# Optimization experiments

Measured on AMD Instinct MI355X. Metric: run time of the kernel, lower is better.

The kernel has to match this reference:

```python
import jax, jax.numpy as jnp
import numpy as np

B, N = 2, 512
D_NODE, D_EDGE, D_HID, H = 128, 64, 128, 8
DH = D_HID // H  # per-head dim = 16
SCALE = 1.0 / (D_HID ** 0.5)  # note: scale uses full d_hid as in source


def setup_inputs() -> dict:
    key = jax.random.key(0)
    k1, k2, k3, k4 = jax.random.split(key, 4)
    node_features = jax.random.normal(k1, (B, N, D_NODE), dtype=jnp.float32)
    edge_features = jax.random.normal(k2, (B, N, N, D_EDGE), dtype=jnp.float32)
    mask = jnp.ones((B, N, N), dtype=bool)
    # Linear weights (stored as (in, out); math identical to torch x @ W.T)
    W_node = jax.random.normal(k3, (D_NODE, 3 * D_HID), dtype=jnp.float32) / np.sqrt(D_NODE)
    W_edge = jax.random.normal(k4, (D_EDGE, 3 * D_HID), dtype=jnp.float32) / np.sqrt(D_EDGE)
    return {"node_features": node_features, "edge_features": edge_features,
            "mask": mask, "W_node": W_node, "W_edge": W_edge}


def _split_heads_node(x):
    # (b, n, h*c) -> (b, h, n, c)
    b, n, hc = x.shape
    return x.reshape(b, n, H, hc // H).transpose(0, 2, 1, 3)


def _split_heads_edge(x):
    # (b, n, m, h*c) -> (b, h, n, m, c)
    b, n, m, hc = x.shape
    return x.reshape(b, n, m, H, hc // H).transpose(0, 3, 1, 2, 4)


def reference(node_features, edge_features, mask, W_node, W_edge):
    # node qkv: (b, n, 3*d_hid) -> (b, h, n, 3*dh) -> chunk
    qkv_n = _split_heads_node(node_features @ W_node)
    q_node, k_node, v_node = jnp.split(qkv_n, 3, axis=-1)  # each (b,h,n,dh)
    # edge qkv: (b, n, n, 3*d_hid) -> (b, h, n, n, 3*dh) -> chunk
    qkv_e = _split_heads_edge(edge_features @ W_edge)
    q_edge, k_edge, v_edge = jnp.split(qkv_e, 3, axis=-1)  # each (b,h,n,n,dh)

    q = q_node[:, :, :, None, :] + q_edge   # (b,h,i,j,dh)
    k = k_node[:, :, None, :, :] + k_edge   # (b,h,i,j,dh)
    v = v_node[:, :, None, :, :] + v_edge   # (b,h,i,j,dh)

    dots = SCALE * jnp.einsum('bhijd,bhijd->bhij', q, k)
    attn = jax.nn.softmax(dots, axis=-1)
    out = jnp.einsum('bhij,bhijd->bhid', attn, v)  # (b,h,n,dh)
    # (b,h,n,dh) -> (b,n,h*dh)
    b, h, n, dh = out.shape
    return out.transpose(0, 2, 1, 3).reshape(b, n, h * dh)
```

## Files before the change

### kernel.cpp

```cpp
#include <hip/hip_runtime.h>

#define NN 512
#define OC 384
#define S2F 0.12751694f

typedef __attribute__((ext_vector_type(8))) short short8;
typedef __attribute__((ext_vector_type(4))) float f32x4;

__device__ __forceinline__ unsigned short f2bf(float x) {
    unsigned u = __builtin_bit_cast(unsigned, x);
    u = (u + 0x7fffu + ((u >> 16) & 1u)) >> 16;
    return (unsigned short)u;
}

__global__ __launch_bounds__(256) void prep0_kernel(
    const float* __restrict__ Wn, const float* __restrict__ We,
    const float* __restrict__ node,
    unsigned short* __restrict__ WtN, unsigned short* __restrict__ WtE,
    unsigned short* __restrict__ nodeBf)
{
    int idx = blockIdx.x * 256 + threadIdx.x;
    if (idx < 24576) {
        int o = idx >> 6, k = idx & 63;
        WtE[idx] = f2bf(We[k * OC + o]);
    } else if (idx < 24576 + 49152) {
        int id = idx - 24576;
        int o = id >> 7, k = id & 127;
        WtN[id] = f2bf(Wn[k * OC + o]);
    } else {
        int id = idx - 73728;
        nodeBf[id] = f2bf(node[id]);
    }
}

__global__ __launch_bounds__(256) void prep1_kernel(
    const unsigned short* __restrict__ nodeBf,
    const unsigned short* __restrict__ WtN,
    float* __restrict__ qnF,
    float* __restrict__ nodeKV)
{
    const int t = threadIdx.x;
    const int w = t >> 6;
    const int lane = t & 63;
    const int lj = lane & 15;
    const int quad = lane >> 4;
    const int nbase = blockIdx.x * 32;

    short8 bfr[2][4];
#pragma unroll
    for (int nt = 0; nt < 2; ++nt)
#pragma unroll
        for (int ks = 0; ks < 4; ++ks)
            bfr[nt][ks] = *reinterpret_cast<const short8*>(
                nodeBf + (size_t)(nbase + nt * 16 + lj) * 128 + ks * 32 + quad * 8);

#pragma unroll
    for (int m = 0; m < 6; ++m) {
        int ot = (6 * w + m) * 16;
        short8 afr[4];
#pragma unroll
        for (int ks = 0; ks < 4; ++ks)
            afr[ks] = *reinterpret_cast<const short8*>(
                WtN + (size_t)(ot + lj) * 128 + ks * 32 + quad * 8);
#pragma unroll
        for (int nt = 0; nt < 2; ++nt) {
            f32x4 acc = {0.f, 0.f, 0.f, 0.f};
#pragma unroll
            for (int ks = 0; ks < 4; ++ks)
                acc = __builtin_amdgcn_mfma_f32_16x16x32_bf16(afr[ks], bfr[nt][ks], acc, 0, 0, 0);
            int n = nbase + nt * 16 + lj;
            int bb = n >> 9, ii = n & 511;
#pragma unroll
            for (int r = 0; r < 4; ++r) {
                int o = ot + quad * 4 + r;
                int h = o / 48, rem = o - h * 48;
                size_t base = (size_t)(bb * 8 + h) * NN + ii;
                if (rem < 16) {
                    qnF[base * 16 + rem] = acc[r];
                } else {
                    int d = (rem - 16) & 15;
                    int isv = (rem >= 32) ? 4 : 0;
                    nodeKV[base * 32 + (d >> 2) * 8 + isv + (d & 3)] = acc[r];
                }
            }
        }
    }
}

__global__ __launch_bounds__(256) void rt_attn_main(
    const float* __restrict__ edge,
    const float* __restrict__ qnF,
    const float* __restrict__ nodeKV,
    const unsigned short* __restrict__ WtE,
    float* __restrict__ out)
{
    __shared__ unsigned short sE[2][64 * 72];
    const int blk = blockIdx.x;
    const int hg = blk & 1;
    const int bi = blk >> 1;
    const int b = bi >> 9;
    const int i = bi & 511;
    const int t = threadIdx.x;
    const int h = hg * 4 + (t >> 6);
    const int lane = t & 63;
    const int lj = lane & 15;
    const int quad = lane >> 4;

    const int sj[4] = { t >> 4, (256 + t) >> 4, (512 + t) >> 4, (768 + t) >> 4 };
    const int sc = (t & 15) * 4;

    const float* eBase = edge + (size_t)bi * NN * 64;
    f32x4 pf[4];
#pragma unroll
    for (int it = 0; it < 4; ++it)
        pf[it] = *reinterpret_cast<const f32x4*>(eBase + (size_t)sj[it] * 64 + sc);

    short8 afr[3][2];
#pragma unroll
    for (int T = 0; T < 3; ++T)
#pragma unroll
        for (int sec = 0; sec < 2; ++sec)
            afr[T][sec] = *reinterpret_cast<const short8*>(
                WtE + (size_t)(h * 48 + T * 16 + lj) * 64 + sec * 32 + quad * 8);

    const f32x4 qn = *reinterpret_cast<const f32x4*>(
        qnF + ((size_t)(b * 8 + h) * NN + i) * 16 + quad * 4);

    float l = 0.f;
    float oa[4] = {0.f, 0.f, 0.f, 0.f};
    const float* kvBase = nodeKV + (size_t)(b * 8 + h) * NN * 32;

    {
#pragma unroll
        for (int it = 0; it < 4; ++it) {
            ushort4 u;
            u.x = f2bf(pf[it][0]); u.y = f2bf(pf[it][1]);
            u.z = f2bf(pf[it][2]); u.w = f2bf(pf[it][3]);
            *reinterpret_cast<ushort4*>(&sE[0][sj[it] * 72 + sc]) = u;
        }
    }
    __syncthreads();

    for (int tt = 0; tt < 8; ++tt) {
        const int cur = tt & 1;
        if (tt < 7) {
            const float* nb = eBase + (size_t)(tt + 1) * 4096;
#pragma unroll
            for (int it = 0; it < 4; ++it)
                pf[it] = *reinterpret_cast<const f32x4*>(nb + (size_t)sj[it] * 64 + sc);
        }
        f32x4 ka[4], va[4];
#pragma unroll
        for (int jn = 0; jn < 4; ++jn) {
            const float* kvp = kvBase + (size_t)(tt * 64 + jn * 16 + lj) * 32 + quad * 8;
            ka[jn] = *reinterpret_cast<const f32x4*>(kvp);
            va[jn] = *reinterpret_cast<const f32x4*>(kvp + 4);
        }
        float dp[4];
        f32x4 fvv[4];
#pragma unroll
        for (int jn = 0; jn < 4; ++jn) {
            const int jrow = jn * 16 + lj;
            short8 b0 = *reinterpret_cast<const short8*>(&sE[cur][jrow * 72 + quad * 8]);
            short8 b1 = *reinterpret_cast<const short8*>(&sE[cur][jrow * 72 + 32 + quad * 8]);
            f32x4 fq = qn;
            f32x4 fk = ka[jn];
            f32x4 fv = va[jn];
            fq = __builtin_amdgcn_mfma_f32_16x16x32_bf16(afr[0][0], b0, fq, 0, 0, 0);
            fq = __builtin_amdgcn_mfma_f32_16x16x32_bf16(afr[0][1], b1, fq, 0, 0, 0);
            fk = __builtin_amdgcn_mfma_f32_16x16x32_bf16(afr[1][0], b0, fk, 0, 0, 0);
            fk = __builtin_amdgcn_mfma_f32_16x16x32_bf16(afr[1][1], b1, fk, 0, 0, 0);
            fv = __builtin_amdgcn_mfma_f32_16x16x32_bf16(afr[2][0], b0, fv, 0, 0, 0);
            fv = __builtin_amdgcn_mfma_f32_16x16x32_bf16(afr[2][1], b1, fv, 0, 0, 0);
            fvv[jn] = fv;
            float d0 = fq[0] * fk[0];
            d0 = fmaf(fq[1], fk[1], d0);
            d0 = fmaf(fq[2], fk[2], d0);
            d0 = fmaf(fq[3], fk[3], d0);
            dp[jn] = d0;
        }
        float t16[4], t32[4], wg[4];
#pragma unroll
        for (int jn = 0; jn < 4; ++jn) t16[jn] = __shfl_xor(dp[jn], 16);
#pragma unroll
        for (int jn = 0; jn < 4; ++jn) dp[jn] += t16[jn];
#pragma unroll
        for (int jn = 0; jn < 4; ++jn) t32[jn] = __shfl_xor(dp[jn], 32);
#pragma unroll
        for (int jn = 0; jn < 4; ++jn) {
            wg[jn] = exp2f((dp[jn] + t32[jn]) * S2F);
            l += wg[jn];
        }
        if (tt < 7) {
#pragma unroll
            for (int it = 0; it < 4; ++it) {
                ushort4 u;
                u.x = f2bf(pf[it][0]); u.y = f2bf(pf[it][1]);
                u.z = f2bf(pf[it][2]); u.w = f2bf(pf[it][3]);
                *reinterpret_cast<ushort4*>(&sE[cur ^ 1][sj[it] * 72 + sc]) = u;
            }
        }
#pragma unroll
        for (int jn = 0; jn < 4; ++jn)
#pragma unroll
            for (int r = 0; r < 4; ++r)
                oa[r] = fmaf(wg[jn], fvv[jn][r], oa[r]);
        if (tt < 7) __syncthreads();
    }

#pragma unroll
    for (int off = 1; off <= 8; off <<= 1) {
        l += __shfl_xor(l, off);
#pragma unroll
        for (int r = 0; r < 4; ++r) oa[r] += __shfl_xor(oa[r], off);
    }
    if (lj == 0) {
        float inv = 1.0f / l;
        f32x4 o4;
#pragma unroll
        for (int r = 0; r < 4; ++r) o4[r] = oa[r] * inv;
        *reinterpret_cast<f32x4*>(out + (size_t)bi * 128 + h * 16 + quad * 4) = o4;
    }
}

extern "C" void kernel_launch(void* const* d_in, const int* in_sizes, int n_in,
                              void* d_out, int out_size, void* d_ws, size_t ws_size,
                              hipStream_t stream) {
    const float* node = (const float*)d_in[0];
    const float* edge = (const float*)d_in[1];
    const float* Wn = (const float*)d_in[3];
    const float* We = (const float*)d_in[4];
    float* out = (float*)d_out;

    char* ws = (char*)d_ws;
    float* qnF = (float*)ws;
    float* nodeKV = (float*)(ws + 524288);
    unsigned short* WtE = (unsigned short*)(ws + 1572864);
    unsigned short* WtN = (unsigned short*)(ws + 1622016);
    unsigned short* nodeBf = (unsigned short*)(ws + 1720320);

    prep0_kernel<<<800, 256, 0, stream>>>(Wn, We, node, WtN, WtE, nodeBf);
    prep1_kernel<<<32, 256, 0, stream>>>(nodeBf, WtN, qnF, nodeKV);
    rt_attn_main<<<2 * 2 * NN, 256, 0, stream>>>(edge, qnF, nodeKV, WtE, out);
}
```

Before: 267.8 us.

## Process all 8 heads per block to halve edge tile loads

Each block now handles one (b,i) row with 512 threads covering all 8 heads, instead of two blocks each loading the same edge row for 4 heads. This halves global reads and bf16 conversion of the edge features, which dominate memory traffic. Each thread now prefetches 2 vectors instead of 4. The conversion uses the packed bf16x2 intrinsic, and the prefetch store is moved after the accumulation. The cost is larger blocks, a launch-bounds change that may limit registers, and fewer blocks in the grid.

Result: faster. 241.6 us (-9.8%).

```diff
diff --git a/kernel.cpp b/kernel.cpp
--- a/kernel.cpp
+++ b/kernel.cpp
@@ -1,4 +1,5 @@
 #include <hip/hip_runtime.h>
+#include <hip/hip_bf16.h>
 
 #define NN 512
 #define OC 384
@@ -11,6 +12,13 @@
     unsigned u = __builtin_bit_cast(unsigned, x);
     u = (u + 0x7fffu + ((u >> 16) & 1u)) >> 16;
     return (unsigned short)u;
+}
+
+__device__ __forceinline__ ushort4 cvt4(f32x4 a) {
+    union { ushort4 u4; __hip_bfloat162 h[2]; } r;
+    r.h[0] = __float22bfloat162_rn(make_float2(a[0], a[1]));
+    r.h[1] = __float22bfloat162_rn(make_float2(a[2], a[3]));
+    return r.u4;
 }
 
 __global__ __launch_bounds__(256) void prep0_kernel(
@@ -87,7 +95,7 @@
     }
 }
 
-__global__ __launch_bounds__(256) void rt_attn_main(
+__global__ __launch_bounds__(512, 4) void rt_attn_main(
     const float* __restrict__ edge,
     const float* __restrict__ qnF,
     const float* __restrict__ nodeKV,
@@ -95,25 +103,23 @@
     float* __restrict__ out)
 {
     __shared__ unsigned short sE[2][64 * 72];
-    const int blk = blockIdx.x;
-    const int hg = blk & 1;
-    const int bi = blk >> 1;
+    const int bi = blockIdx.x;
     const int b = bi >> 9;
     const int i = bi & 511;
     const int t = threadIdx.x;
-    const int h = hg * 4 + (t >> 6);
+    const int h = t >> 6;
     const int lane = t & 63;
     const int lj = lane & 15;
     const int quad = lane >> 4;
 
-    const int sj[4] = { t >> 4, (256 + t) >> 4, (512 + t) >> 4, (768 + t) >> 4 };
+    const int sj0 = t >> 4;
+    const int sj1 = sj0 + 32;
     const int sc = (t & 15) * 4;
 
     const float* eBase = edge + (size_t)bi * NN * 64;
-    f32x4 pf[4];
-#pragma unroll
-    for (int it = 0; it < 4; ++it)
-        pf[it] = *reinterpret_cast<const f32x4*>(eBase + (size_t)sj[it] * 64 + sc);
+    f32x4 pf0, pf1;
+    pf0 = *reinterpret_cast<const f32x4*>(eBase + (size_t)sj0 * 64 + sc);
+    pf1 = *reinterpret_cast<const f32x4*>(eBase + (size_t)sj1 * 64 + sc);
 
     short8 afr[3][2];
 #pragma unroll
@@ -131,30 +137,24 @@
     const float* kvBase = nodeKV + (size_t)(b * 8 + h) * NN * 32;
 
     {
-#pragma unroll
-        for (int it = 0; it < 4; ++it) {
-            ushort4 u;
-            u.x = f2bf(pf[it][0]); u.y = f2bf(pf[it][1]);
-            u.z = f2bf(pf[it][2]); u.w = f2bf(pf[it][3]);
-            *reinterpret_cast<ushort4*>(&sE[0][sj[it] * 72 + sc]) = u;
-        }
+        *reinterpret_cast<ushort4*>(&sE[0][sj0 * 72 + sc]) = cvt4(pf0);
+        *reinterpret_cast<ushort4*>(&sE[0][sj1 * 72 + sc]) = cvt4(pf1);
     }
     __syncthreads();
 
     for (int tt = 0; tt < 8; ++tt) {
         const int cur = tt & 1;
-        if (tt < 7) {
-            const float* nb = eBase + (size_t)(tt + 1) * 4096;
-#pragma unroll
-            for (int it = 0; it < 4; ++it)
-                pf[it] = *reinterpret_cast<const f32x4*>(nb + (size_t)sj[it] * 64 + sc);
-        }
         f32x4 ka[4], va[4];
 #pragma unroll
         for (int jn = 0; jn < 4; ++jn) {
             const float* kvp = kvBase + (size_t)(tt * 64 + jn * 16 + lj) * 32 + quad * 8;
             ka[jn] = *reinterpret_cast<const f32x4*>(kvp);
             va[jn] = *reinterpret_cast<const f32x4*>(kvp + 4);
+        }
+        if (tt < 7) {
+            const float* nb = eBase + (size_t)(tt + 1) * 4096;
+            pf0 = *reinterpret_cast<const f32x4*>(nb + (size_t)sj0 * 64 + sc);
+            pf1 = *reinterpret_cast<const f32x4*>(nb + (size_t)sj1 * 64 + sc);
         }
         float dp[4];
         f32x4 fvv[4];
@@ -164,12 +164,12 @@
             short8 b0 = *reinterpret_cast<const short8*>(&sE[cur][jrow * 72 + quad * 8]);
             short8 b1 = *reinterpret_cast<const short8*>(&sE[cur][jrow * 72 + 32 + quad * 8]);
             f32x4 fq = qn;
-            f32x4 fk = ka[jn];
-            f32x4 fv = va[jn];
             fq = __builtin_amdgcn_mfma_f32_16x16x32_bf16(afr[0][0], b0, fq, 0, 0, 0);
             fq = __builtin_amdgcn_mfma_f32_16x16x32_bf16(afr[0][1], b1, fq, 0, 0, 0);
+            f32x4 fk = ka[jn];
             fk = __builtin_amdgcn_mfma_f32_16x16x32_bf16(afr[1][0], b0, fk, 0, 0, 0);
             fk = __builtin_amdgcn_mfma_f32_16x16x32_bf16(afr[1][1], b1, fk, 0, 0, 0);
+            f32x4 fv = va[jn];
             fv = __builtin_amdgcn_mfma_f32_16x16x32_bf16(afr[2][0], b0, fv, 0, 0, 0);
             fv = __builtin_amdgcn_mfma_f32_16x16x32_bf16(afr[2][1], b1, fv, 0, 0, 0);
             fvv[jn] = fv;
@@ -191,21 +191,16 @@
             wg[jn] = exp2f((dp[jn] + t32[jn]) * S2F);
             l += wg[jn];
         }
-        if (tt < 7) {
-#pragma unroll
-            for (int it = 0; it < 4; ++it) {
-                ushort4 u;
-                u.x = f2bf(pf[it][0]); u.y = f2bf(pf[it][1]);
-                u.z = f2bf(pf[it][2]); u.w = f2bf(pf[it][3]);
-                *reinterpret_cast<ushort4*>(&sE[cur ^ 1][sj[it] * 72 + sc]) = u;
-            }
-        }
 #pragma unroll
         for (int jn = 0; jn < 4; ++jn)
 #pragma unroll
             for (int r = 0; r < 4; ++r)
                 oa[r] = fmaf(wg[jn], fvv[jn][r], oa[r]);
-        if (tt < 7) __syncthreads();
+        if (tt < 7) {
+            *reinterpret_cast<ushort4*>(&sE[cur ^ 1][sj0 * 72 + sc]) = cvt4(pf0);
+            *reinterpret_cast<ushort4*>(&sE[cur ^ 1][sj1 * 72 + sc]) = cvt4(pf1);
+            __syncthreads();
+        }
     }
 
 #pragma unroll
@@ -241,5 +236,5 @@
 
     prep0_kernel<<<800, 256, 0, stream>>>(Wn, We, node, WtN, WtE, nodeBf);
     prep1_kernel<<<32, 256, 0, stream>>>(nodeBf, WtN, qnF, nodeKV);
-    rt_attn_main<<<2 * 2 * NN, 256, 0, stream>>>(edge, qnF, nodeKV, WtE, out);
-}
+    rt_attn_main<<<2 * NN, 512, 0, stream>>>(edge, qnF, nodeKV, WtE, out);
+}
```
